# Kernel tuning notes

Hardware: AMD Instinct MI355X
Metric: run time of the kernel (lower is better)

Reference implementation:

```python
import jax, jax.numpy as jnp
import numpy as np

# 4D conv over (L, P, W, H) decomposed as k shifted 3D convs over (P, W, H),
# with the L spatial dim folded into the batch. Faithful to convNd(num_dims=4),
# stride 1, 'same' padding (padding = (k-1)//2), no bias.

def conv4d(x, w):
    # x: [B, C, L, P, W, H]; w: [O, I, k, k, k, k]
    k = w.shape[2]
    p = (k - 1) // 2
    B, C, L, P, Wd, Hd = x.shape
    O = w.shape[0]
    xp = jnp.pad(x, ((0, 0), (0, 0), (p, p), (0, 0), (0, 0), (0, 0)))
    dn = ('NCDHW', 'OIDHW', 'NCDHW')
    out = jnp.zeros((B, O, L, P, Wd, Hd), x.dtype)
    for dl in range(k):  # k <= 3, static loop over kernel taps along L
        xs = xp[:, :, dl:dl + L]                                  # [B,C,L,P,W,H]
        xs = xs.transpose(0, 2, 1, 3, 4, 5).reshape(B * L, C, P, Wd, Hd)
        y = jax.lax.conv_general_dilated(xs, w[:, :, dl], (1, 1, 1),
                                         [(p, p)] * 3, dimension_numbers=dn)
        out = out + y.reshape(B, L, O, P, Wd, Hd).transpose(0, 2, 1, 3, 4, 5)
    return out


def inception4d(x, weights):
    # mean over parallel 4D convs with kernel sizes 1, 3, ... (2i+1)
    acc = conv4d(x, weights[0])
    for w in weights[1:]:
        acc = acc + conv4d(x, w)
    return acc / len(weights)


def setup_inputs() -> dict:
    key = jax.random.key(0)
    ks = jax.random.split(key, 5)
    B, T, W, H, C = 4, 48, 8, 8, 32
    d_model, d_ff = 32, 64
    x = jax.random.normal(ks[0], (B, T, W, H, C), dtype=jnp.float32)
    # Inception_Block4D weights: kernel sizes 1 and 3 (num_kernels=2), no bias
    w1_0 = jax.random.normal(ks[1], (d_ff, d_model, 1, 1, 1, 1), dtype=jnp.float32) * 0.1
    w1_1 = jax.random.normal(ks[2], (d_ff, d_model, 3, 3, 3, 3), dtype=jnp.float32) * 0.02
    w2_0 = jax.random.normal(ks[3], (d_model, d_ff, 1, 1, 1, 1), dtype=jnp.float32) * 0.1
    w2_1 = jax.random.normal(ks[4], (d_model, d_ff, 3, 3, 3, 3), dtype=jnp.float32) * 0.02
    return {"x": x, "w1_0": w1_0, "w1_1": w1_1, "w2_0": w2_0, "w2_1": w2_1}


def reference(x, w1_0, w1_1, w2_0, w2_1):
    B, T, W, H, C = x.shape
    periods = (2, 3, 4)                       # FFT_for_Period hardcoded output
    xf = jnp.ones((B, len(periods)), x.dtype) # hardcoded uniform weights
    real_len = T                              # seq_len + pred_len
    res = []
    for period in periods:
        if real_len % period != 0:
            length = (real_len // period + 1) * period
            out = jnp.concatenate([x, x[:, -(length - real_len):]], axis=1)
        else:
            length = real_len
            out = x
        # [B, L, P, W, H, C] -> [B, C, L, P, W, H]
        out = out.reshape(B, length // period, period, W, H, C).transpose(0, 5, 1, 2, 3, 4)
        h = inception4d(out, [w1_0, w1_1])
        h = jax.nn.gelu(h, approximate=False)  # torch nn.GELU default (exact)
        h = inception4d(h, [w2_0, w2_1])
        # [B, C, L, P, W, H] -> [B, (L P), W, H, C]
        h = h.transpose(0, 2, 3, 4, 5, 1).reshape(B, length, W, H, C)
        res.append(h[:, :real_len])
    res = jnp.stack(res, axis=1)              # [B, k, T, W, H, C]
    pw = jax.nn.softmax(xf, axis=1).reshape(B, len(periods), 1, 1, 1, 1)
    return jnp.sum(res * pw, axis=1) + x
```

## Files before the change

### kernel.cpp

```cpp
#include <hip/hip_runtime.h>
#include <math.h>


typedef __attribute__((ext_vector_type(8))) short bf16x8;
typedef __attribute__((ext_vector_type(4))) float f32x4;
typedef unsigned short u16;

#define XC 3200
#define HC2 7168
#define XSEG 617600
#define ZSEG_END 639104
#define W1OFF 639104
#define W2OFF 804992
#define H1OFF 970880
#define H1P 1383424
#define PREP_N 970880
#define OUT_Q 98304
#define PREP_TOT (PREP_N + OUT_Q)

#define WAITVM(N) asm volatile("s_waitcnt vmcnt(" #N ")" ::: "memory")
#define SBAR()    asm volatile("s_barrier" ::: "memory")

__device__ __forceinline__ u16 f2bf(float f) {
    unsigned u = __float_as_uint(f);
    unsigned r = u + 0x7fffu + ((u >> 16) & 1u);
    return (u16)(r >> 16);
}
__device__ __forceinline__ float gelu_exact(float v) {
    return 0.5f * v * (1.0f + erff(v * 0.7071067811865476f));
}

__device__ __forceinline__ void cp1k(const u16* g, u16* l, int lane) {
    __builtin_amdgcn_global_load_lds(
        (const __attribute__((address_space(1))) unsigned int*)(g + lane * 8),
        (__attribute__((address_space(3))) unsigned int*)(l + lane * 8),
        16, 0, 0);
}

__global__ __launch_bounds__(256) void prep(
    const float* __restrict__ x,
    const float* __restrict__ w1_0, const float* __restrict__ w1_1,
    const float* __restrict__ w2_0, const float* __restrict__ w2_1,
    u16* __restrict__ ws, float* __restrict__ out) {
    int i = blockIdx.x * 256 + threadIdx.x;
    if (i < XSEG) {
        int cellidx = i / XC; int inner = i - cellidx * XC;
        int cellpos = inner >> 5; int low = inner & 31;
        int sc = low >> 3, jj = low & 7;
        int c = ((sc ^ (cellpos & 3)) << 3) + jj;
        int wp = cellpos / 10, hp = cellpos - (cellpos / 10) * 10;
        float v = 0.f;
        if (cellidx < 192 && wp >= 1 && wp <= 8 && hp >= 1 && hp <= 8)
            v = x[(cellidx * 64 + (wp - 1) * 8 + (hp - 1)) * 32 + c];
        ws[i] = f2bf(v);
    } else if (i < ZSEG_END) {
        int j = i - XSEG;
        int per = j / 7168; int off = j - per * 7168;
        ws[H1OFF + per * H1P + 192 * 7168 + off] = 0;
    } else if (i < W2OFF) {
        int j = i - W1OFF;
        int tap = j >> 11; int r = j & 2047;
        int nh = r >> 10; int rr = r & 1023;
        int chunkh = rr >> 3, jj = rr & 7;
        int m = chunkh & 15, nq = (chunkh >> 4) & 1, quad = chunkh >> 5;
        int o = nh * 32 + nq * 16 + m, c = quad * 8 + jj;
        float v = 0.5f * w1_1[(o * 32 + c) * 81 + tap];
        if (tap == 40) v += 0.5f * w1_0[o * 32 + c];
        ws[i] = f2bf(v);
    } else if (i < PREP_N) {
        int j = i - W2OFF;
        int tap = j >> 11; int r = j & 2047;
        int kh = r >> 10; int rr = r & 1023;
        int chunkh = rr >> 3, jj = rr & 7;
        int m = chunkh & 15, nt = (chunkh >> 4) & 1, quad = chunkh >> 5;
        int o = nt * 16 + m, c = kh * 32 + quad * 8 + jj;
        float v = 0.5f * w2_1[(o * 64 + c) * 81 + tap];
        if (tap == 40) v += 0.5f * w2_0[o * 64 + c];
        ws[i] = f2bf(v);
    } else if (i < PREP_TOT) {
        int j = i - PREP_N;
        ((float4*)out)[j] = ((const float4*)x)[j];
    }
}

template<int P>
__device__ __forceinline__ int cidx(int bb, int l2, int q2) {
    constexpr int L = 48 / P;
    return ((unsigned)l2 < (unsigned)L && (unsigned)q2 < (unsigned)P)
               ? bb * 48 + l2 * P + q2 : 192;
}

template<int P>
__device__ __forceinline__ void conv1_body(
    const u16* __restrict__ xs, const u16* __restrict__ w1b,
    u16* __restrict__ h1, int tp, int bb, int nh,
    u16* __restrict__ s_a) {
    constexpr int HB = (P == 2) ? 0 : (P == 3) ? H1P : 2 * H1P;

    int tid = threadIdx.x;
    int lane = tid & 63, wv = tid >> 6;
    int m = lane & 15, quad = lane >> 4;
    int tloc = wv >> 1, mh = wv & 1;

    int t0 = tp * 2, t1 = tp * 2 + 1;
    int l0 = t0 / P, q0 = t0 - l0 * P;
    int l1 = t1 / P, q1 = t1 - l1 * P;

    int sp[2];
#pragma unroll
    for (int mtl = 0; mtl < 2; ++mtl) {
        int pos = (mh * 2 + mtl) * 16 + m;
        sp[mtl] = (pos >> 3) * 10 + (pos & 7);
    }

    f32x4 acc[2][2];
#pragma unroll
    for (int mtl = 0; mtl < 2; ++mtl)
#pragma unroll
        for (int nq = 0; nq < 2; ++nq) acc[mtl][nq] = f32x4{0.f, 0.f, 0.f, 0.f};

    const u16* wlane = w1b + nh * 1024 + ((quad * 32 + m) << 3);

    auto stageA = [&](int gg) {
        int dl = gg / 3, dq = gg - (gg / 3) * 3;
        const u16* c0 = xs + cidx<P>(bb, l0 + dl - 1, q0 + dq - 1) * XC;
        const u16* c1 = xs + cidx<P>(bb, l1 + dl - 1, q1 + dq - 1) * XC;
#pragma unroll
        for (int i = 0; i < 4; ++i) {
            int k = wv * 4 + i; if (k >= 14) k = 13;
            int cell = k / 7, pc = k - (k / 7) * 7;
            cp1k((cell ? c1 : c0) + pc * 512,
                 s_a + (cell * 2 + (gg & 1)) * 3584 + pc * 512, lane);
        }
    };

    stageA(0);
    WAITVM(0); SBAR();

#pragma unroll 1
    for (int gg = 0; gg < 9; ++gg) {
        if (gg < 8) stageA(gg + 1);

        const u16* ba = s_a + (tloc * 2 + (gg & 1)) * 3584;
        const u16* wgg = wlane + gg * 9 * 2048;
#pragma unroll
        for (int pj = 0; pj < 9; ++pj) {
            int part = pj / 3, j = pj - (pj / 3) * 3;
            const u16* tw = wgg + pj * 2048;
            bf16x8 wf[2];
            wf[0] = *(const bf16x8*)(tw);
            wf[1] = *(const bf16x8*)(tw + 128);
            bf16x8 af[2];
#pragma unroll
            for (int mtl = 0; mtl < 2; ++mtl) {
                int cellpos = sp[mtl] + part * 10 + j;
                af[mtl] = *(const bf16x8*)(ba + cellpos * 32 +
                                           ((quad ^ (cellpos & 3)) << 3));
            }
#pragma unroll
            for (int mtl = 0; mtl < 2; ++mtl)
#pragma unroll
                for (int nq = 0; nq < 2; ++nq)
                    acc[mtl][nq] = __builtin_amdgcn_mfma_f32_16x16x32_bf16(
                        af[mtl], wf[nq], acc[mtl][nq], 0, 0, 0);
        }
        if (gg < 8) { WAITVM(0); SBAR(); }
    }

    int t = tp * 2 + tloc;
    u16* hh = h1 + HB + (bb * 48 + t) * HC2 + nh * 3584;
#pragma unroll
    for (int mtl = 0; mtl < 2; ++mtl)
#pragma unroll
        for (int r = 0; r < 4; ++r) {
            int pos = (mh * 2 + mtl) * 16 + quad * 4 + r;
            int cellpos = ((pos >> 3) + 1) * 10 + (pos & 7) + 1;
#pragma unroll
            for (int nq = 0; nq < 2; ++nq) {
                int ol = nq * 16 + m;
                hh[cellpos * 32 + (((ol >> 3) ^ (cellpos & 3)) << 3) + (ol & 7)] =
                    f2bf(gelu_exact(acc[mtl][nq][r]));
            }
        }
#pragma unroll
    for (int it = 0; it < 5; ++it) {
        int k = it * 256 + tid;
        if (k < 1152) {
            int tb = k >= 576; int rr = k - tb * 576;
            int bp = rr >> 4, u = rr & 15;
            int cp;
            if (bp < 10) cp = bp;
            else if (bp < 20) cp = 90 + (bp - 10);
            else if (bp < 28) cp = (bp - 19) * 10;
            else cp = (bp - 27) * 10 + 9;
            unsigned int* h32 = (unsigned int*)(h1 + HB +
                (bb * 48 + tp * 2 + tb) * HC2 + nh * 3584);
            h32[cp * 16 + u] = 0;
        }
    }
}

__global__ __launch_bounds__(256, 4) void conv1_k(
    const u16* __restrict__ ws_x, const u16* __restrict__ ws_w1,
    u16* __restrict__ ws_h1) {
    __shared__ __align__(16) u16 s_a[4 * 3584];
    int g = blockIdx.x;
    int jid = (g & 7) * 72 + (g >> 3);
    int per = jid / 192; int rem = jid - per * 192;
    int bb = rem / 48; int r2 = rem - bb * 48;
    int tp = r2 >> 1, nh = r2 & 1;
    if (per == 0)      conv1_body<2>(ws_x, ws_w1, ws_h1, tp, bb, nh, s_a);
    else if (per == 1) conv1_body<3>(ws_x, ws_w1, ws_h1, tp, bb, nh, s_a);
    else               conv1_body<4>(ws_x, ws_w1, ws_h1, tp, bb, nh, s_a);
}

template<int P>
__device__ __forceinline__ void conv2_body(
    const u16* __restrict__ h1, const u16* __restrict__ w2b,
    float* __restrict__ out, int tp, int bb, int kh,
    u16* __restrict__ s_a) {
    constexpr int HB = (P == 2) ? 0 : (P == 3) ? H1P : 2 * H1P;

    int tid = threadIdx.x;
    int lane = tid & 63, wv = tid >> 6;
    int m = lane & 15, quad = lane >> 4;
    int tloc = wv >> 1, mh = wv & 1;

    int t0 = tp * 2, t1 = tp * 2 + 1;
    int l0 = t0 / P, q0 = t0 - l0 * P;
    int l1 = t1 / P, q1 = t1 - l1 * P;
    const u16* hb = h1 + HB;

    int sp[2];
#pragma unroll
    for (int mtl = 0; mtl < 2; ++mtl) {
        int pos = (mh * 2 + mtl) * 16 + m;
        sp[mtl] = (pos >> 3) * 10 + (pos & 7);
    }

    f32x4 acc[2][2];
#pragma unroll
    for (int mtl = 0; mtl < 2; ++mtl)
#pragma unroll
        for (int nt = 0; nt < 2; ++nt) acc[mtl][nt] = f32x4{0.f, 0.f, 0.f, 0.f};

    const u16* wlane = w2b + kh * 1024 + ((quad * 32 + m) << 3);

    auto stageA = [&](int gg) {
        int dl = gg / 3, dq = gg - (gg / 3) * 3;
        const u16* c0 = hb + cidx<P>(bb, l0 + dl - 1, q0 + dq - 1) * HC2 + kh * 3584;
        const u16* c1 = hb + cidx<P>(bb, l1 + dl - 1, q1 + dq - 1) * HC2 + kh * 3584;
#pragma unroll
        for (int i = 0; i < 4; ++i) {
            int k = wv * 4 + i; if (k >= 14) k = 13;
            int cell = k / 7, pc = k - (k / 7) * 7;
            cp1k((cell ? c1 : c0) + pc * 512,
                 s_a + (cell * 2 + (gg & 1)) * 3584 + pc * 512, lane);
        }
    };

    stageA(0);
    WAITVM(0); SBAR();

#pragma unroll 1
    for (int gg = 0; gg < 9; ++gg) {
        if (gg < 8) stageA(gg + 1);

        const u16* ba = s_a + (tloc * 2 + (gg & 1)) * 3584;
        const u16* wgg = wlane + gg * 9 * 2048;
#pragma unroll
        for (int pj = 0; pj < 9; ++pj) {
            int part = pj / 3, j = pj - (pj / 3) * 3;
            const u16* tw = wgg + pj * 2048;
            bf16x8 wf[2];
            wf[0] = *(const bf16x8*)(tw);
            wf[1] = *(const bf16x8*)(tw + 128);
            bf16x8 af[2];
#pragma unroll
            for (int mtl = 0; mtl < 2; ++mtl) {
                int cellpos = sp[mtl] + part * 10 + j;
                af[mtl] = *(const bf16x8*)(ba + cellpos * 32 +
                                           ((quad ^ (cellpos & 3)) << 3));
            }
#pragma unroll
            for (int mtl = 0; mtl < 2; ++mtl)
#pragma unroll
                for (int nt = 0; nt < 2; ++nt)
                    acc[mtl][nt] = __builtin_amdgcn_mfma_f32_16x16x32_bf16(
                        af[mtl], wf[nt], acc[mtl][nt], 0, 0, 0);
        }
        if (gg < 8) { WAITVM(0); SBAR(); }
    }

    int t = tp * 2 + tloc;
    float* orow = out + (bb * 48 + t) * 2048;
    const float s = 1.0f / 3.0f;
#pragma unroll
    for (int mtl = 0; mtl < 2; ++mtl)
#pragma unroll
        for (int nt = 0; nt < 2; ++nt)
#pragma unroll
            for (int r = 0; r < 4; ++r) {
                int pos = (mh * 2 + mtl) * 16 + quad * 4 + r;
                atomicAdd(&orow[pos * 32 + nt * 16 + m], acc[mtl][nt][r] * s);
            }
}

__global__ __launch_bounds__(256, 4) void conv2_k(
    const u16* __restrict__ ws_h1, const u16* __restrict__ ws_w2,
    float* __restrict__ out) {
    __shared__ __align__(16) u16 s_a[4 * 3584];
    int g = blockIdx.x;
    int jid = (g & 7) * 72 + (g >> 3);
    int per = jid / 192; int rem = jid - per * 192;
    int bb = rem / 48; int r2 = rem - bb * 48;
    int tp = r2 >> 1, kh = r2 & 1;
    if (per == 0)      conv2_body<2>(ws_h1, ws_w2, out, tp, bb, kh, s_a);
    else if (per == 1) conv2_body<3>(ws_h1, ws_w2, out, tp, bb, kh, s_a);
    else               conv2_body<4>(ws_h1, ws_w2, out, tp, bb, kh, s_a);
}

extern "C" void kernel_launch(void* const* d_in, const int* in_sizes, int n_in,
                              void* d_out, int out_size, void* d_ws, size_t ws_size,
                              hipStream_t stream) {
    const float* x    = (const float*)d_in[0];
    const float* w1_0 = (const float*)d_in[1];
    const float* w1_1 = (const float*)d_in[2];
    const float* w2_0 = (const float*)d_in[3];
    const float* w2_1 = (const float*)d_in[4];
    float* out = (float*)d_out;

    u16* ws = (u16*)d_ws;
    u16* ws_x  = ws;
    u16* ws_w1 = ws + W1OFF;
    u16* ws_w2 = ws + W2OFF;
    u16* ws_h1 = ws + H1OFF;

    prep<<<(PREP_TOT + 255) / 256, 256, 0, stream>>>(
        x, w1_0, w1_1, w2_0, w2_1, ws, out);
    conv1_k<<<576, 256, 0, stream>>>(ws_x, ws_w1, ws_h1);
    conv2_k<<<576, 256, 0, stream>>>(ws_h1, ws_w2, out);
}
```

Measured before the change: 131.1 us.

## Stage weights in LDS, use 128-thread blocks with one time step per wave

Each conv block now runs 2 waves instead of 4. Each wave owns one time step and all 64 spatial positions, so it holds 4x2 MFMA accumulators. Per-tap weight slices are copied into shared memory once per block rather than each lane reading them from global memory. The double-buffered prefetch of the input cells is removed, so each of the 9 taps now loads and then waits synchronously, which gives up load/compute overlap. The intent is to cut redundant global weight traffic and improve MFMA operand reuse, at the cost of less latency hiding and fewer waves per block.

```diff
diff --git a/kernel.cpp b/kernel.cpp
--- a/kernel.cpp
+++ b/kernel.cpp
@@ -94,86 +94,72 @@
 __device__ __forceinline__ void conv1_body(
     const u16* __restrict__ xs, const u16* __restrict__ w1b,
     u16* __restrict__ h1, int tp, int bb, int nh,
-    u16* __restrict__ s_a) {
+    u16* __restrict__ s_a, u16* __restrict__ s_w) {
     constexpr int HB = (P == 2) ? 0 : (P == 3) ? H1P : 2 * H1P;
 
     int tid = threadIdx.x;
     int lane = tid & 63, wv = tid >> 6;
     int m = lane & 15, quad = lane >> 4;
-    int tloc = wv >> 1, mh = wv & 1;
-
-    int t0 = tp * 2, t1 = tp * 2 + 1;
-    int l0 = t0 / P, q0 = t0 - l0 * P;
-    int l1 = t1 / P, q1 = t1 - l1 * P;
-
-    int sp[2];
-#pragma unroll
-    for (int mtl = 0; mtl < 2; ++mtl) {
-        int pos = (mh * 2 + mtl) * 16 + m;
+    int t0 = tp * 2, t = t0 + wv;
+    int l = t / P, q = t - l * P;
+
+    int sp[4];
+#pragma unroll
+    for (int mtl = 0; mtl < 4; ++mtl) {
+        int pos = mtl * 16 + m;
         sp[mtl] = (pos >> 3) * 10 + (pos & 7);
     }
 
-    f32x4 acc[2][2];
-#pragma unroll
-    for (int mtl = 0; mtl < 2; ++mtl)
+    f32x4 acc[4][2];
+#pragma unroll
+    for (int mtl = 0; mtl < 4; ++mtl)
 #pragma unroll
         for (int nq = 0; nq < 2; ++nq) acc[mtl][nq] = f32x4{0.f, 0.f, 0.f, 0.f};
 
-    const u16* wlane = w1b + nh * 1024 + ((quad * 32 + m) << 3);
-
-    auto stageA = [&](int gg) {
-        int dl = gg / 3, dq = gg - (gg / 3) * 3;
-        const u16* c0 = xs + cidx<P>(bb, l0 + dl - 1, q0 + dq - 1) * XC;
-        const u16* c1 = xs + cidx<P>(bb, l1 + dl - 1, q1 + dq - 1) * XC;
-#pragma unroll
-        for (int i = 0; i < 4; ++i) {
-            int k = wv * 4 + i; if (k >= 14) k = 13;
-            int cell = k / 7, pc = k - (k / 7) * 7;
-            cp1k((cell ? c1 : c0) + pc * 512,
-                 s_a + (cell * 2 + (gg & 1)) * 3584 + pc * 512, lane);
-        }
-    };
-
-    stageA(0);
-    WAITVM(0); SBAR();
+    const u16* ba = s_a + wv * 3584;
 
 #pragma unroll 1
-    for (int gg = 0; gg < 9; ++gg) {
-        if (gg < 8) stageA(gg + 1);
-
-        const u16* ba = s_a + (tloc * 2 + (gg & 1)) * 3584;
-        const u16* wgg = wlane + gg * 9 * 2048;
+    for (int g = 0; g < 9; ++g) {
+        int dl = g / 3, dq = g - dl * 3;
+        const u16* ac = xs + cidx<P>(bb, l + dl - 1, q + dq - 1) * XC;
+        u16* ad = s_a + wv * 3584;
+#pragma unroll
+        for (int i = 0; i < 7; ++i)
+            cp1k(ac + i * 512, ad + i * 512, lane);
+#pragma unroll
+        for (int i = 0; i < 9; ++i) {
+            int k = wv * 9 + i;
+            cp1k(w1b + (g * 9 + (k >> 1)) * 2048 + nh * 1024 + (k & 1) * 512,
+                 s_w + k * 512, lane);
+        }
+        WAITVM(0); SBAR();
+
 #pragma unroll
         for (int pj = 0; pj < 9; ++pj) {
-            int part = pj / 3, j = pj - (pj / 3) * 3;
-            const u16* tw = wgg + pj * 2048;
-            bf16x8 wf[2];
-            wf[0] = *(const bf16x8*)(tw);
-            wf[1] = *(const bf16x8*)(tw + 128);
-            bf16x8 af[2];
-#pragma unroll
-            for (int mtl = 0; mtl < 2; ++mtl) {
-                int cellpos = sp[mtl] + part * 10 + j;
-                af[mtl] = *(const bf16x8*)(ba + cellpos * 32 +
-                                           ((quad ^ (cellpos & 3)) << 3));
+            int dw = pj / 3, dh = pj - (pj / 3) * 3;
+            const u16* tw = s_w + pj * 1024;
+            bf16x8 wf0 = *(const bf16x8*)(tw + (((quad * 2 + 0) * 16 + m) << 3));
+            bf16x8 wf1 = *(const bf16x8*)(tw + (((quad * 2 + 1) * 16 + m) << 3));
+#pragma unroll
+            for (int mtl = 0; mtl < 4; ++mtl) {
+                int cellpos = sp[mtl] + dw * 10 + dh;
+                bf16x8 af = *(const bf16x8*)(ba + cellpos * 32 +
+                                             ((quad ^ (cellpos & 3)) << 3));
+                acc[mtl][0] = __builtin_amdgcn_mfma_f32_16x16x32_bf16(
+                    af, wf0, acc[mtl][0], 0, 0, 0);
+                acc[mtl][1] = __builtin_amdgcn_mfma_f32_16x16x32_bf16(
+                    af, wf1, acc[mtl][1], 0, 0, 0);
             }
-#pragma unroll
-            for (int mtl = 0; mtl < 2; ++mtl)
-#pragma unroll
-                for (int nq = 0; nq < 2; ++nq)
-                    acc[mtl][nq] = __builtin_amdgcn_mfma_f32_16x16x32_bf16(
-                        af[mtl], wf[nq], acc[mtl][nq], 0, 0, 0);
-        }
-        if (gg < 8) { WAITVM(0); SBAR(); }
-    }
-
-    int t = tp * 2 + tloc;
+        }
+        if (g < 8) SBAR();
+    }
+
     u16* hh = h1 + HB + (bb * 48 + t) * HC2 + nh * 3584;
 #pragma unroll
-    for (int mtl = 0; mtl < 2; ++mtl)
+    for (int mtl = 0; mtl < 4; ++mtl)
 #pragma unroll
         for (int r = 0; r < 4; ++r) {
-            int pos = (mh * 2 + mtl) * 16 + quad * 4 + r;
+            int pos = mtl * 16 + quad * 4 + r;
             int cellpos = ((pos >> 3) + 1) * 10 + (pos & 7) + 1;
 #pragma unroll
             for (int nq = 0; nq < 2; ++nq) {
@@ -183,141 +169,128 @@
             }
         }
 #pragma unroll
-    for (int it = 0; it < 5; ++it) {
-        int k = it * 256 + tid;
-        if (k < 1152) {
-            int tb = k >= 576; int rr = k - tb * 576;
-            int bp = rr >> 4, u = rr & 15;
-            int cp;
-            if (bp < 10) cp = bp;
-            else if (bp < 20) cp = 90 + (bp - 10);
-            else if (bp < 28) cp = (bp - 19) * 10;
-            else cp = (bp - 27) * 10 + 9;
-            unsigned int* h32 = (unsigned int*)(h1 + HB +
-                (bb * 48 + tp * 2 + tb) * HC2 + nh * 3584);
-            h32[cp * 16 + u] = 0;
-        }
-    }
-}
-
-__global__ __launch_bounds__(256, 4) void conv1_k(
+    for (int it = 0; it < 9; ++it) {
+        int k = it * 128 + tid;
+        int tb = k >= 576; int rr = k - tb * 576;
+        int bp = rr >> 4, u = rr & 15;
+        int cp;
+        if (bp < 10) cp = bp;
+        else if (bp < 20) cp = 90 + (bp - 10);
+        else if (bp < 28) cp = (bp - 19) * 10;
+        else cp = (bp - 27) * 10 + 9;
+        unsigned int* h32 = (unsigned int*)(h1 + HB +
+            (bb * 48 + t0 + tb) * HC2 + nh * 3584);
+        h32[cp * 16 + u] = 0;
+    }
+}
+
+__global__ __launch_bounds__(128, 2) void conv1_k(
     const u16* __restrict__ ws_x, const u16* __restrict__ ws_w1,
     u16* __restrict__ ws_h1) {
-    __shared__ __align__(16) u16 s_a[4 * 3584];
+    __shared__ __align__(16) u16 s_a[2 * 3584];
+    __shared__ __align__(16) u16 s_w[18 * 512];
     int g = blockIdx.x;
     int jid = (g & 7) * 72 + (g >> 3);
     int per = jid / 192; int rem = jid - per * 192;
     int bb = rem / 48; int r2 = rem - bb * 48;
     int tp = r2 >> 1, nh = r2 & 1;
-    if (per == 0)      conv1_body<2>(ws_x, ws_w1, ws_h1, tp, bb, nh, s_a);
-    else if (per == 1) conv1_body<3>(ws_x, ws_w1, ws_h1, tp, bb, nh, s_a);
-    else               conv1_body<4>(ws_x, ws_w1, ws_h1, tp, bb, nh, s_a);
+    if (per == 0)      conv1_body<2>(ws_x, ws_w1, ws_h1, tp, bb, nh, s_a, s_w);
+    else if (per == 1) conv1_body<3>(ws_x, ws_w1, ws_h1, tp, bb, nh, s_a, s_w);
+    else               conv1_body<4>(ws_x, ws_w1, ws_h1, tp, bb, nh, s_a, s_w);
 }
 
 template<int P>
 __device__ __forceinline__ void conv2_body(
     const u16* __restrict__ h1, const u16* __restrict__ w2b,
     float* __restrict__ out, int tp, int bb, int kh,
-    u16* __restrict__ s_a) {
+    u16* __restrict__ s_a, u16* __restrict__ s_w) {
     constexpr int HB = (P == 2) ? 0 : (P == 3) ? H1P : 2 * H1P;
 
     int tid = threadIdx.x;
     int lane = tid & 63, wv = tid >> 6;
     int m = lane & 15, quad = lane >> 4;
-    int tloc = wv >> 1, mh = wv & 1;
-
-    int t0 = tp * 2, t1 = tp * 2 + 1;
-    int l0 = t0 / P, q0 = t0 - l0 * P;
-    int l1 = t1 / P, q1 = t1 - l1 * P;
+    int t0 = tp * 2, t = t0 + wv;
+    int l = t / P, q = t - l * P;
     const u16* hb = h1 + HB;
 
-    int sp[2];
-#pragma unroll
-    for (int mtl = 0; mtl < 2; ++mtl) {
-        int pos = (mh * 2 + mtl) * 16 + m;
+    int sp[4];
+#pragma unroll
+    for (int mtl = 0; mtl < 4; ++mtl) {
+        int pos = mtl * 16 + m;
         sp[mtl] = (pos >> 3) * 10 + (pos & 7);
     }
 
-    f32x4 acc[2][2];
-#pragma unroll
-    for (int mtl = 0; mtl < 2; ++mtl)
+    f32x4 acc[4][2];
+#pragma unroll
+    for (int mtl = 0; mtl < 4; ++mtl)
 #pragma unroll
         for (int nt = 0; nt < 2; ++nt) acc[mtl][nt] = f32x4{0.f, 0.f, 0.f, 0.f};
 
-    const u16* wlane = w2b + kh * 1024 + ((quad * 32 + m) << 3);
-
-    auto stageA = [&](int gg) {
-        int dl = gg / 3, dq = gg - (gg / 3) * 3;
-        const u16* c0 = hb + cidx<P>(bb, l0 + dl - 1, q0 + dq - 1) * HC2 + kh * 3584;
-        const u16* c1 = hb + cidx<P>(bb, l1 + dl - 1, q1 + dq - 1) * HC2 + kh * 3584;
-#pragma unroll
-        for (int i = 0; i < 4; ++i) {
-            int k = wv * 4 + i; if (k >= 14) k = 13;
-            int cell = k / 7, pc = k - (k / 7) * 7;
-            cp1k((cell ? c1 : c0) + pc * 512,
-                 s_a + (cell * 2 + (gg & 1)) * 3584 + pc * 512, lane);
-        }
-    };
-
-    stageA(0);
-    WAITVM(0); SBAR();
+    const u16* ba = s_a + wv * 3584;
 
 #pragma unroll 1
-    for (int gg = 0; gg < 9; ++gg) {
-        if (gg < 8) stageA(gg + 1);
-
-        const u16* ba = s_a + (tloc * 2 + (gg & 1)) * 3584;
-        const u16* wgg = wlane + gg * 9 * 2048;
+    for (int g = 0; g < 9; ++g) {
+        int dl = g / 3, dq = g - dl * 3;
+        const u16* ac = hb + cidx<P>(bb, l + dl - 1, q + dq - 1) * HC2 +
+                        kh * 3584;
+        u16* ad = s_a + wv * 3584;
+#pragma unroll
+        for (int i = 0; i < 7; ++i)
+            cp1k(ac + i * 512, ad + i * 512, lane);
+#pragma unroll
+        for (int i = 0; i < 9; ++i) {
+            int k = wv * 9 + i;
+            cp1k(w2b + (g * 9 + (k >> 1)) * 2048 + kh * 1024 + (k & 1) * 512,
+                 s_w + k * 512, lane);
+        }
+        WAITVM(0); SBAR();
+
 #pragma unroll
         for (int pj = 0; pj < 9; ++pj) {
-            int part = pj / 3, j = pj - (pj / 3) * 3;
-            const u16* tw = wgg + pj * 2048;
-            bf16x8 wf[2];
-            wf[0] = *(const bf16x8*)(tw);
-            wf[1] = *(const bf16x8*)(tw + 128);
-            bf16x8 af[2];
-#pragma unroll
-            for (int mtl = 0; mtl < 2; ++mtl) {
-                int cellpos = sp[mtl] + part * 10 + j;
-                af[mtl] = *(const bf16x8*)(ba + cellpos * 32 +
-                                           ((quad ^ (cellpos & 3)) << 3));
+            int dw = pj / 3, dh = pj - (pj / 3) * 3;
+            const u16* tw = s_w + pj * 1024;
+            bf16x8 wf0 = *(const bf16x8*)(tw + (((quad * 2 + 0) * 16 + m) << 3));
+            bf16x8 wf1 = *(const bf16x8*)(tw + (((quad * 2 + 1) * 16 + m) << 3));
+#pragma unroll
+            for (int mtl = 0; mtl < 4; ++mtl) {
+                int cellpos = sp[mtl] + dw * 10 + dh;
+                bf16x8 af = *(const bf16x8*)(ba + cellpos * 32 +
+                                             ((quad ^ (cellpos & 3)) << 3));
+                acc[mtl][0] = __builtin_amdgcn_mfma_f32_16x16x32_bf16(
+                    af, wf0, acc[mtl][0], 0, 0, 0);
+                acc[mtl][1] = __builtin_amdgcn_mfma_f32_16x16x32_bf16(
+                    af, wf1, acc[mtl][1], 0, 0, 0);
             }
-#pragma unroll
-            for (int mtl = 0; mtl < 2; ++mtl)
-#pragma unroll
-                for (int nt = 0; nt < 2; ++nt)
-                    acc[mtl][nt] = __builtin_amdgcn_mfma_f32_16x16x32_bf16(
-                        af[mtl], wf[nt], acc[mtl][nt], 0, 0, 0);
-        }
-        if (gg < 8) { WAITVM(0); SBAR(); }
-    }
-
-    int t = tp * 2 + tloc;
+        }
+        if (g < 8) SBAR();
+    }
+
     float* orow = out + (bb * 48 + t) * 2048;
     const float s = 1.0f / 3.0f;
 #pragma unroll
-    for (int mtl = 0; mtl < 2; ++mtl)
+    for (int mtl = 0; mtl < 4; ++mtl)
 #pragma unroll
         for (int nt = 0; nt < 2; ++nt)
 #pragma unroll
             for (int r = 0; r < 4; ++r) {
-                int pos = (mh * 2 + mtl) * 16 + quad * 4 + r;
+                int pos = mtl * 16 + quad * 4 + r;
                 atomicAdd(&orow[pos * 32 + nt * 16 + m], acc[mtl][nt][r] * s);
             }
 }
 
-__global__ __launch_bounds__(256, 4) void conv2_k(
+__global__ __launch_bounds__(128, 2) void conv2_k(
     const u16* __restrict__ ws_h1, const u16* __restrict__ ws_w2,
     float* __restrict__ out) {
-    __shared__ __align__(16) u16 s_a[4 * 3584];
+    __shared__ __align__(16) u16 s_a[2 * 3584];
+    __shared__ __align__(16) u16 s_w[18 * 512];
     int g = blockIdx.x;
     int jid = (g & 7) * 72 + (g >> 3);
     int per = jid / 192; int rem = jid - per * 192;
     int bb = rem / 48; int r2 = rem - bb * 48;
     int tp = r2 >> 1, kh = r2 & 1;
-    if (per == 0)      conv2_body<2>(ws_h1, ws_w2, out, tp, bb, kh, s_a);
-    else if (per == 1) conv2_body<3>(ws_h1, ws_w2, out, tp, bb, kh, s_a);
-    else               conv2_body<4>(ws_h1, ws_w2, out, tp, bb, kh, s_a);
+    if (per == 0)      conv2_body<2>(ws_h1, ws_w2, out, tp, bb, kh, s_a, s_w);
+    else if (per == 1) conv2_body<3>(ws_h1, ws_w2, out, tp, bb, kh, s_a, s_w);
+    else               conv2_body<4>(ws_h1, ws_w2, out, tp, bb, kh, s_a, s_w);
 }
 
 extern "C" void kernel_launch(void* const* d_in, const int* in_sizes, int n_in,
@@ -338,6 +311,6 @@
 
     prep<<<(PREP_TOT + 255) / 256, 256, 0, stream>>>(
         x, w1_0, w1_1, w2_0, w2_1, ws, out);
-    conv1_k<<<576, 256, 0, stream>>>(ws_x, ws_w1, ws_h1);
-    conv2_k<<<576, 256, 0, stream>>>(ws_h1, ws_w2, out);
-}
+    conv1_k<<<576, 128, 0, stream>>>(ws_x, ws_w1, ws_h1);
+    conv2_k<<<576, 128, 0, stream>>>(ws_h1, ws_w2, out);
+}
```

Result: faster. 121.3 us (-7.5%).
